# Performance work log

Hardware: AMD Instinct MI355X
Metric: run time of the kernel (lower is better)

The kernel has to match this reference:

```python
import jax, jax.numpy as jnp
import numpy as np
import math

B, S, H, D = 2, 2048, 16, 64  # batch, seq, heads, head_dim (hidden=1024)


def setup_inputs() -> dict:
    key = jax.random.key(0)
    kq, kk, kv, kb, km = jax.random.split(key, 5)
    q = jax.random.normal(kq, (B, S, H, D), dtype=jnp.float32)
    k = jax.random.normal(kk, (B, S, H, D), dtype=jnp.float32)
    v = jax.random.normal(kv, (B, S, H, D), dtype=jnp.float32)
    attn_bias = jax.random.normal(kb, (B, H, S, S), dtype=jnp.float32)
    mask = jax.random.randint(km, (B, S, S), 0, 2).astype(jnp.bool_)
    return {"q": q, "k": k, "v": v, "attn_bias": attn_bias, "mask": mask}


def reference(q, k, v, attn_bias, mask):
    # Faithful to CoreAttention: q is MULTIPLIED by sqrt(d_head),
    # masked positions in the score matrix are filled with 0 (not -inf),
    # dropout rate is 0 (identity).
    scale = math.sqrt(D)
    # scores: [B, H, S, S]
    x = jnp.einsum('bshd,bthd->bhst', q * scale, k)
    x = x + attn_bias
    x = jnp.where(mask[:, None, :, :], jnp.float32(0.0), x)  # masked_fill(mask, 0)
    x = jax.nn.softmax(x, axis=-1)
    out = jnp.einsum('bhst,bthd->bshd', x, v)  # [B, S, H, D]
    return out.reshape(B, S, H * D)
```

## Files before the change

### kernel.cpp

```cpp
#include <hip/hip_runtime.h>
#include <math.h>


namespace {
constexpr int Bn = 2, Sn = 2048, Hn = 16, Dn = 64;
constexpr int QT = 64;
constexpr int KT = 64;
constexpr int ST = 72;

typedef _Float16 f16x8 __attribute__((ext_vector_type(8)));
typedef float    f32x4 __attribute__((ext_vector_type(4)));
}

__global__ __launch_bounds__(256, 4)
void core_attn_kernel(const float* __restrict__ Q,
                      const float* __restrict__ K,
                      const float* __restrict__ V,
                      const float* __restrict__ Bias,
                      const int*   __restrict__ Mask,
                      float* __restrict__ Out)
{
    const int qt = blockIdx.x;
    const int h  = blockIdx.y;
    const int b  = blockIdx.z;
    const int q0 = qt * QT;

    const int tid  = threadIdx.x;
    const int wave = tid >> 6;
    const int lane = tid & 63;
    const int c    = lane & 15;
    const int quad = lane >> 4;

    __shared__ __align__(16) _Float16 Khi[KT * ST];
    __shared__ __align__(16) _Float16 Klo[KT * ST];
    __shared__ __align__(16) _Float16 Vt [Dn * ST];
    __shared__ __align__(16) _Float16 Pl [4][16 * ST];

    f16x8 qhi[2], qlo[2];
    {
        const int qrow = q0 + wave * 16 + c;
        const float* qp = Q + ((size_t)((b * Sn + qrow) * Hn + h)) * Dn + quad * 8;
        #pragma unroll
        for (int kc = 0; kc < 2; ++kc) {
            float4 v0 = *(const float4*)(qp + kc * 32);
            float4 v1 = *(const float4*)(qp + kc * 32 + 4);
            float buf[8] = {v0.x, v0.y, v0.z, v0.w, v1.x, v1.y, v1.z, v1.w};
            #pragma unroll
            for (int j = 0; j < 8; ++j) {
                float f = buf[j] * 8.0f;
                _Float16 hi = (_Float16)f;
                qhi[kc][j] = hi;
                qlo[kc][j] = (_Float16)(f - (float)hi);
            }
        }
    }

    f32x4 Oa[4];
    float m_i[4], l_i[4];
    #pragma unroll
    for (int r = 0; r < 4; ++r) { m_i[r] = -INFINITY; l_i[r] = 0.0f; }
    #pragma unroll
    for (int t = 0; t < 4; ++t) Oa[t] = (f32x4){0.f, 0.f, 0.f, 0.f};

    const float* bias_row = Bias + ((size_t)(b * Hn + h) * Sn + (q0 + wave * 16 + quad * 4)) * Sn;
    const int*   mask_row = Mask + ((size_t)(b * Sn + (q0 + wave * 16 + quad * 4))) * Sn;

    const int srow = tid >> 2;
    const int dseg = (tid & 3) * 16;
    const float* kbase = K + ((size_t)((b * Sn + srow) * Hn + h)) * Dn + dseg;
    const float* vbase = V + ((size_t)((b * Sn + srow) * Hn + h)) * Dn + dseg;

    for (int k0 = 0; k0 < Sn; k0 += KT) {
        __syncthreads();
        {
            const float* kp = kbase + (size_t)k0 * (Hn * Dn);
            const float* vp = vbase + (size_t)k0 * (Hn * Dn);
            float4 kv[4], vv[4];
            #pragma unroll
            for (int i = 0; i < 4; ++i) kv[i] = *(const float4*)(kp + 4 * i);
            #pragma unroll
            for (int i = 0; i < 4; ++i) vv[i] = *(const float4*)(vp + 4 * i);
            f16x8 khiv[2], klov[2];
            const float* kf = (const float*)kv;
            #pragma unroll
            for (int j = 0; j < 16; ++j) {
                float f = kf[j];
                _Float16 hi = (_Float16)f;
                khiv[j >> 3][j & 7] = hi;
                klov[j >> 3][j & 7] = (_Float16)(f - (float)hi);
            }
            *(f16x8*)&Khi[srow * ST + dseg]     = khiv[0];
            *(f16x8*)&Khi[srow * ST + dseg + 8] = khiv[1];
            *(f16x8*)&Klo[srow * ST + dseg]     = klov[0];
            *(f16x8*)&Klo[srow * ST + dseg + 8] = klov[1];
            const float* vf = (const float*)vv;
            #pragma unroll
            for (int j = 0; j < 16; ++j)
                Vt[(dseg + j) * ST + srow] = (_Float16)vf[j];
        }
        __syncthreads();

        float sc[4][4];
        #pragma unroll
        for (int ct = 0; ct < 4; ++ct) {
            f32x4 acc;
            #pragma unroll
            for (int r = 0; r < 4; ++r)
                acc[r] = bias_row[(size_t)r * Sn + k0 + ct * 16 + c];
            #pragma unroll
            for (int kc = 0; kc < 2; ++kc) {
                f16x8 kh = *(const f16x8*)&Khi[(ct * 16 + c) * ST + kc * 32 + quad * 8];
                f16x8 kl = *(const f16x8*)&Klo[(ct * 16 + c) * ST + kc * 32 + quad * 8];
                acc = __builtin_amdgcn_mfma_f32_16x16x32_f16(qhi[kc], kh, acc, 0, 0, 0);
                acc = __builtin_amdgcn_mfma_f32_16x16x32_f16(qhi[kc], kl, acc, 0, 0, 0);
                acc = __builtin_amdgcn_mfma_f32_16x16x32_f16(qlo[kc], kh, acc, 0, 0, 0);
            }
            #pragma unroll
            for (int r = 0; r < 4; ++r) {
                int mv = mask_row[(size_t)r * Sn + k0 + ct * 16 + c];
                sc[ct][r] = mv ? 0.0f : acc[r];
            }
        }

        float mt[4];
        #pragma unroll
        for (int r = 0; r < 4; ++r)
            mt[r] = fmaxf(fmaxf(sc[0][r], sc[1][r]), fmaxf(sc[2][r], sc[3][r]));
        #pragma unroll
        for (int off = 8; off >= 1; off >>= 1) {
            #pragma unroll
            for (int r = 0; r < 4; ++r)
                mt[r] = fmaxf(mt[r], __shfl_xor(mt[r], off, 64));
        }
        float alpha[4], rs[4];
        #pragma unroll
        for (int r = 0; r < 4; ++r) {
            float mn = fmaxf(m_i[r], mt[r]);
            alpha[r] = __expf(m_i[r] - mn);
            m_i[r] = mn;
            rs[r] = 0.0f;
        }
        #pragma unroll
        for (int ct = 0; ct < 4; ++ct) {
            #pragma unroll
            for (int r = 0; r < 4; ++r) {
                float p = __expf(sc[ct][r] - m_i[r]);
                sc[ct][r] = p;
                rs[r] += p;
            }
        }
        #pragma unroll
        for (int off = 8; off >= 1; off >>= 1) {
            #pragma unroll
            for (int r = 0; r < 4; ++r)
                rs[r] += __shfl_xor(rs[r], off, 64);
        }
        #pragma unroll
        for (int r = 0; r < 4; ++r)
            l_i[r] = l_i[r] * alpha[r] + rs[r];
        #pragma unroll
        for (int t = 0; t < 4; ++t) {
            #pragma unroll
            for (int r = 0; r < 4; ++r)
                Oa[t][r] *= alpha[r];
        }

        #pragma unroll
        for (int ct = 0; ct < 4; ++ct) {
            #pragma unroll
            for (int r = 0; r < 4; ++r)
                Pl[wave][(quad * 4 + r) * ST + ct * 16 + c] = (_Float16)sc[ct][r];
        }
        f16x8 pf[2];
        #pragma unroll
        for (int kc = 0; kc < 2; ++kc)
            pf[kc] = *(const f16x8*)&Pl[wave][c * ST + kc * 32 + quad * 8];

        #pragma unroll
        for (int td = 0; td < 4; ++td) {
            #pragma unroll
            for (int kc = 0; kc < 2; ++kc) {
                f16x8 vfrag = *(const f16x8*)&Vt[(td * 16 + c) * ST + kc * 32 + quad * 8];
                Oa[td] = __builtin_amdgcn_mfma_f32_16x16x32_f16(pf[kc], vfrag, Oa[td], 0, 0, 0);
            }
        }
    }

    #pragma unroll
    for (int r = 0; r < 4; ++r) l_i[r] = 1.0f / l_i[r];
    float* op = Out + ((size_t)(b * Sn + q0 + wave * 16 + quad * 4)) * (Hn * Dn) + h * Dn + c;
    #pragma unroll
    for (int td = 0; td < 4; ++td) {
        #pragma unroll
        for (int r = 0; r < 4; ++r)
            op[(size_t)r * (Hn * Dn) + td * 16] = Oa[td][r] * l_i[r];
    }
}

extern "C" void kernel_launch(void* const* d_in, const int* in_sizes, int n_in,
                              void* d_out, int out_size, void* d_ws, size_t ws_size,
                              hipStream_t stream) {
    const float* q    = (const float*)d_in[0];
    const float* k    = (const float*)d_in[1];
    const float* v    = (const float*)d_in[2];
    const float* bias = (const float*)d_in[3];
    const int*   mask = (const int*)d_in[4];
    float* out = (float*)d_out;

    dim3 grid(Sn / QT, Hn, Bn);
    core_attn_kernel<<<grid, 256, 0, stream>>>(q, k, v, bias, mask, out);
}
```

Before: 915.4 us.

## Prefetch next K/V/bias tile into registers during current tile compute

Loads the next iteration's K, V and bias values into registers while the current tile's MFMAs and softmax run, hiding global-memory latency behind compute. The K/V staging thread mapping changes so each wave covers 64 consecutive rows per 16-column segment. The first barrier is moved to the end of the loop, and mask values are loaded before the score MFMAs. This costs extra VGPRs (about 48 more live floats) and may reduce occupancy under launch_bounds(256,4).

```diff
diff --git a/kernel.cpp b/kernel.cpp
--- a/kernel.cpp
+++ b/kernel.cpp
@@ -65,23 +65,30 @@
     const float* bias_row = Bias + ((size_t)(b * Hn + h) * Sn + (q0 + wave * 16 + quad * 4)) * Sn;
     const int*   mask_row = Mask + ((size_t)(b * Sn + (q0 + wave * 16 + quad * 4))) * Sn;
 
-    const int srow = tid >> 2;
-    const int dseg = (tid & 3) * 16;
+    const int srow = tid & 63;
+    const int dseg = (tid >> 6) * 16;
     const float* kbase = K + ((size_t)((b * Sn + srow) * Hn + h)) * Dn + dseg;
     const float* vbase = V + ((size_t)((b * Sn + srow) * Hn + h)) * Dn + dseg;
 
+    float4 kPre[4], vPre[4];
+    float  biasPre[16];
+
+    {
+        #pragma unroll
+        for (int i = 0; i < 4; ++i) kPre[i] = *(const float4*)(kbase + 4 * i);
+        #pragma unroll
+        for (int i = 0; i < 4; ++i) vPre[i] = *(const float4*)(vbase + 4 * i);
+        #pragma unroll
+        for (int ct = 0; ct < 4; ++ct)
+            #pragma unroll
+            for (int r = 0; r < 4; ++r)
+                biasPre[ct * 4 + r] = bias_row[(size_t)r * Sn + ct * 16 + c];
+    }
+
     for (int k0 = 0; k0 < Sn; k0 += KT) {
-        __syncthreads();
         {
-            const float* kp = kbase + (size_t)k0 * (Hn * Dn);
-            const float* vp = vbase + (size_t)k0 * (Hn * Dn);
-            float4 kv[4], vv[4];
-            #pragma unroll
-            for (int i = 0; i < 4; ++i) kv[i] = *(const float4*)(kp + 4 * i);
-            #pragma unroll
-            for (int i = 0; i < 4; ++i) vv[i] = *(const float4*)(vp + 4 * i);
+            const float* kf = (const float*)kPre;
             f16x8 khiv[2], klov[2];
-            const float* kf = (const float*)kv;
             #pragma unroll
             for (int j = 0; j < 16; ++j) {
                 float f = kf[j];
@@ -93,20 +100,46 @@
             *(f16x8*)&Khi[srow * ST + dseg + 8] = khiv[1];
             *(f16x8*)&Klo[srow * ST + dseg]     = klov[0];
             *(f16x8*)&Klo[srow * ST + dseg + 8] = klov[1];
-            const float* vf = (const float*)vv;
+            const float* vf = (const float*)vPre;
             #pragma unroll
             for (int j = 0; j < 16; ++j)
                 Vt[(dseg + j) * ST + srow] = (_Float16)vf[j];
         }
         __syncthreads();
 
+        f32x4 accv[4];
+        #pragma unroll
+        for (int ct = 0; ct < 4; ++ct)
+            #pragma unroll
+            for (int r = 0; r < 4; ++r)
+                accv[ct][r] = biasPre[ct * 4 + r];
+
+        int mcur[16];
+        #pragma unroll
+        for (int ct = 0; ct < 4; ++ct)
+            #pragma unroll
+            for (int r = 0; r < 4; ++r)
+                mcur[ct * 4 + r] = mask_row[(size_t)r * Sn + k0 + ct * 16 + c];
+
+        const int kn = k0 + KT;
+        if (kn < Sn) {
+            const float* kp = kbase + (size_t)kn * (Hn * Dn);
+            const float* vp = vbase + (size_t)kn * (Hn * Dn);
+            #pragma unroll
+            for (int i = 0; i < 4; ++i) kPre[i] = *(const float4*)(kp + 4 * i);
+            #pragma unroll
+            for (int i = 0; i < 4; ++i) vPre[i] = *(const float4*)(vp + 4 * i);
+            #pragma unroll
+            for (int ct = 0; ct < 4; ++ct)
+                #pragma unroll
+                for (int r = 0; r < 4; ++r)
+                    biasPre[ct * 4 + r] = bias_row[(size_t)r * Sn + kn + ct * 16 + c];
+        }
+
         float sc[4][4];
         #pragma unroll
         for (int ct = 0; ct < 4; ++ct) {
-            f32x4 acc;
-            #pragma unroll
-            for (int r = 0; r < 4; ++r)
-                acc[r] = bias_row[(size_t)r * Sn + k0 + ct * 16 + c];
+            f32x4 acc = accv[ct];
             #pragma unroll
             for (int kc = 0; kc < 2; ++kc) {
                 f16x8 kh = *(const f16x8*)&Khi[(ct * 16 + c) * ST + kc * 32 + quad * 8];
@@ -116,10 +149,8 @@
                 acc = __builtin_amdgcn_mfma_f32_16x16x32_f16(qlo[kc], kh, acc, 0, 0, 0);
             }
             #pragma unroll
-            for (int r = 0; r < 4; ++r) {
-                int mv = mask_row[(size_t)r * Sn + k0 + ct * 16 + c];
-                sc[ct][r] = mv ? 0.0f : acc[r];
-            }
+            for (int r = 0; r < 4; ++r)
+                sc[ct][r] = mcur[ct * 4 + r] ? 0.0f : acc[r];
         }
 
         float mt[4];
@@ -184,6 +215,7 @@
                 Oa[td] = __builtin_amdgcn_mfma_f32_16x16x32_f16(pf[kc], vfrag, Oa[td], 0, 0, 0);
             }
         }
+        __syncthreads();
     }
 
     #pragma unroll
```

New measurement: 1.120 ms. 22.4% more time.
